# Kernel optimization log

Hardware: AMD Instinct MI355X
Metric: run time of the kernel (lower is better)

The kernel has to match this reference:

```python
import jax, jax.numpy as jnp
import numpy as np

N_HEADS = 4
LEAKY_SLOPE = 0.2


def setup_inputs() -> dict:
    key = jax.random.key(0)
    k1, k2, k3 = jax.random.split(key, 3)
    b, c, h, w = 8, 64, 128, 128
    z = jax.random.normal(k1, (b, c, h, w), dtype=jnp.float32)
    # torch.nn.Linear weights are (out_features, in_features); scale ~1/sqrt(fan_in)
    W_Q = jax.random.normal(k2, (c, c), dtype=jnp.float32) * 0.125
    W_K = jax.random.normal(k3, (c, c), dtype=jnp.float32) * 0.125
    return {"z": z, "W_Q": W_Q, "W_K": W_K}


def _axial_branch(z_perm_flat, z_raw_flat, W_Q, W_K, n_batch, seq, d_k, scale):
    # z_perm_flat: (n_batch, seq, c)  -- rearranged input fed to W_Q
    # z_raw_flat : (n_batch, seq, c)  -- raw memory-order reshape fed to W_K
    Q = jnp.matmul(z_perm_flat, W_Q.T).reshape(N_HEADS * n_batch, d_k, seq)
    V = jnp.matmul(z_raw_flat, W_K.T).reshape(N_HEADS * n_batch, d_k, seq)
    # QK-less scores: Q^T Q / sqrt(d_k)  -> (N, seq, seq)
    scores = jnp.einsum('nds,ndt->nst', Q, Q) * scale
    attn = jax.nn.softmax(scores, axis=-1)
    # right-multiply attention onto V, then LeakyReLU
    ctx = jnp.einsum('nds,nst->ndt', V, attn)
    return jax.nn.leaky_relu(ctx, negative_slope=LEAKY_SLOPE)


def reference(z, W_Q, W_K):
    b, c, h, w = z.shape
    d_k = c // N_HEADS
    scale = 1.0 / np.sqrt(d_k).astype(np.float32)

    # Branch 1 (attention over w): a = rearrange 'b c h w -> (b h) w c'
    a = jnp.transpose(z, (0, 2, 3, 1)).reshape(b * h, w, c)
    v1_in = z.reshape(b * h, w, c)  # raw reshape, as in the torch code
    context1 = _axial_branch(a, v1_in, W_Q, W_K, b * h, w, d_k, scale)

    # Branch 2 (attention over h): m = rearrange 'b c h w -> (b w) h c'
    m = jnp.transpose(z, (0, 3, 2, 1)).reshape(b * w, h, c)
    v2_in = z.reshape(b * w, h, c)  # raw reshape, as in the torch code
    context2 = _axial_branch(m, v2_in, W_Q, W_K, b * w, h, d_k, scale)

    context = context1 + context2  # requires h == w
    return context.reshape(b, c, h, w)
```

## Files before the change

kernel.cpp:

```cpp
#include <hip/hip_runtime.h>


typedef __attribute__((ext_vector_type(8))) short bh8;
typedef __attribute__((ext_vector_type(4))) float f32x4;
typedef unsigned short u16;
typedef unsigned int u32;

#define MFMA16(a,b,c) __builtin_amdgcn_mfma_f32_16x16x32_bf16(a,b,c,0,0,0)

#define AIMG_ST 72
#define QP_ST   40
#define V_ST    136
#define PT_ST   72

#define OFF_AH   0
#define OFF_AL   4608
#define OFF_PT   0
#define OFF_QP   18432
#define OFF_VH   28672
#define OFF_VL   33024
#define LDS_TOT  37376

__device__ __forceinline__ void split3(float f, u16& h, u16& l) {
    u32 u = __float_as_uint(f);
    u32 hf = u & 0xFFFF0000u;
    float r = f - __uint_as_float(hf);
    h = (u16)(hf >> 16);
    l = (u16)((__float_as_uint(r) + 0x8000u) >> 16);
}
__device__ __forceinline__ void split2pk(float f0, float f1, u32& hp, u32& lp) {
    u32 u0 = __float_as_uint(f0), u1 = __float_as_uint(f1);
    u32 h0 = u0 & 0xFFFF0000u,  h1 = u1 & 0xFFFF0000u;
    float r0 = f0 - __uint_as_float(h0);
    float r1 = f1 - __uint_as_float(h1);
    hp = (h0 >> 16) | h1;
    lp = ((__float_as_uint(r0) + 0x8000u) >> 16) | ((__float_as_uint(r1) + 0x8000u) & 0xFFFF0000u);
}
__device__ __forceinline__ float lrelu(float x) { return x > 0.f ? x : 0.2f * x; }

__global__ void split_w_kernel(const float* __restrict__ Wq,
                               const float* __restrict__ Wk,
                               u16* __restrict__ ws)
{
    const int i = blockIdx.x * 256 + threadIdx.x;
    const int j = i & 4095;
    const float f = (i < 4096) ? Wq[j] : Wk[j];
    const int base = (i < 4096) ? 0 : 8192;
    u16 h, l; split3(f, h, l);
    ws[base + j] = h;
    ws[base + 4096 + j] = l;
}

template<int MODE>
__device__ __forceinline__ void gemm_in(const u16* Ah, const u16* Al,
                                        bh8 h0a, bh8 h0b, bh8 l0a, bh8 l0b,
                                        bh8 h1a, bh8 h1b, bh8 l1a, bh8 l1b,
                                        u16* o0, u16* o1,
                                        int miQ, int niA, int lid, int quad)
{
    const int offA = (miQ*16 + lid)*AIMG_ST + quad*8;
    bh8 ah0 = *(const bh8*)(Ah + offA);
    bh8 ah1 = *(const bh8*)(Ah + offA + 32);
    bh8 al0 = *(const bh8*)(Al + offA);
    bh8 al1 = *(const bh8*)(Al + offA + 32);
    f32x4 acc0 = {0.f,0.f,0.f,0.f}, acc1 = {0.f,0.f,0.f,0.f};
    acc0 = MFMA16(ah0, h0a, acc0); acc0 = MFMA16(ah0, l0a, acc0); acc0 = MFMA16(al0, h0a, acc0);
    acc0 = MFMA16(ah1, h0b, acc0); acc0 = MFMA16(ah1, l0b, acc0); acc0 = MFMA16(al1, h0b, acc0);
    acc1 = MFMA16(ah0, h1a, acc1); acc1 = MFMA16(ah0, l1a, acc1); acc1 = MFMA16(al0, h1a, acc1);
    acc1 = MFMA16(ah1, h1b, acc1); acc1 = MFMA16(ah1, l1b, acc1); acc1 = MFMA16(al1, h1b, acc1);
    #pragma unroll
    for (int r = 0; r < 4; ++r) {
        const int l = miQ*16 + quad*4 + r;
        const int d = l >> 1;
        const int sbase = (l & 1) << 6;
        {
            const int s = sbase + (niA + 0)*16 + lid;
            u16 h, lo; split3(MODE == 0 ? 0.5f*acc0[r] : acc0[r], h, lo);
            if (MODE == 0) { o0[s*QP_ST + d] = h; o0[s*QP_ST + 16 + d] = lo; }
            else           { o0[d*V_ST + s] = h; o1[d*V_ST + s] = lo; }
        }
        {
            const int s = sbase + (niA + 1)*16 + lid;
            u16 h, lo; split3(MODE == 0 ? 0.5f*acc1[r] : acc1[r], h, lo);
            if (MODE == 0) { o0[s*QP_ST + d] = h; o0[s*QP_ST + 16 + d] = lo; }
            else           { o0[d*V_ST + s] = h; o1[d*V_ST + s] = lo; }
        }
    }
}

__device__ __forceinline__ void branch_attn(const u16* Qp, const u16* Vh, const u16* Vl,
                                            u16* PT, f32x4& cacc0, f32x4& cacc1,
                                            int w, int lid, int quad)
{
    const f32x4 z4 = {0.f, 0.f, 0.f, 0.f};
    cacc0 = z4; cacc1 = z4;
    for (int round = 0; round < 2; ++round) {
        const int rowS = (round*4 + w)*16 + lid;
        const u16* arow = Qp + rowS*QP_ST;
        bh8 a1 = *(const bh8*)(arow + quad*8);
        bh8 a2 = *(const bh8*)(arow + ((quad >= 2) ? (quad-2)*8 : 0));
        bh8 zzv = a2 ^ a2;
        a2 = (quad < 2) ? zzv : a2;
        f32x4 g[8];
        #pragma unroll
        for (int ti = 0; ti < 8; ++ti) {
            const u16* brow = Qp + (ti*16 + lid)*QP_ST;
            bh8 b1 = *(const bh8*)(brow + (quad & 1)*8);
            bh8 b2 = *(const bh8*)(brow + quad*8);
            f32x4 acc = z4;
            acc = MFMA16(a1, b1, acc);
            acc = MFMA16(a2, b2, acc);
            g[ti] = acc;
        }
        float sm[4] = {0.f, 0.f, 0.f, 0.f};
        #pragma unroll
        for (int ti = 0; ti < 8; ++ti)
        #pragma unroll
        for (int r = 0; r < 4; ++r) {
            const float p = __expf(g[ti][r]);
            g[ti][r] = p; sm[r] += p;
        }
        #pragma unroll
        for (int r = 0; r < 4; ++r) {
            float ss = sm[r];
            ss += __shfl_xor(ss, 1); ss += __shfl_xor(ss, 2);
            ss += __shfl_xor(ss, 4); ss += __shfl_xor(ss, 8);
            sm[r] = 1.0f / ss;
        }
        #pragma unroll
        for (int ti = 0; ti < 8; ++ti) {
            const u32 r0 = __float_as_uint(g[ti][0]*sm[0]) + 0x8000u;
            const u32 r1 = __float_as_uint(g[ti][1]*sm[1]) + 0x8000u;
            const u32 r2 = __float_as_uint(g[ti][2]*sm[2]) + 0x8000u;
            const u32 r3 = __float_as_uint(g[ti][3]*sm[3]) + 0x8000u;
            u32* dst = (u32*)(PT + (ti*16 + lid)*PT_ST + w*16 + quad*4);
            dst[0] = (r0 >> 16) | (r1 & 0xFFFF0000u);
            dst[1] = (r2 >> 16) | (r3 & 0xFFFF0000u);
        }
        __syncthreads();
        #pragma unroll
        for (int tj2 = 0; tj2 < 2; ++tj2) {
            const int tj = 2*w + tj2;
            f32x4 acc = tj2 ? cacc1 : cacc0;
            #pragma unroll
            for (int ks = 0; ks < 2; ++ks) {
                bh8 pa = *(const bh8*)(PT + (tj*16 + lid)*PT_ST + ks*32 + quad*8);
                const int vo = lid*V_ST + round*64 + ks*32 + quad*8;
                bh8 vh8 = *(const bh8*)(Vh + vo);
                bh8 vl8 = *(const bh8*)(Vl + vo);
                acc = MFMA16(pa, vh8, acc);
                acc = MFMA16(pa, vl8, acc);
            }
            if (tj2) cacc1 = acc; else cacc0 = acc;
        }
        __syncthreads();
    }
}

#define WOFF(n, ks) (((n)*16 + lid)*64 + (ks)*32 + quad*8)

__global__ __launch_bounds__(256, 4)
void axial_attn_mfma(const float* __restrict__ z, const u16* __restrict__ wsu,
                     float* __restrict__ out)
{
    __shared__ __align__(16) unsigned char lds[LDS_TOT];
    u16* const ptAh = (u16*)(lds + OFF_AH);
    u16* const ptAl = (u16*)(lds + OFF_AL);
    u16* const ptPT = (u16*)(lds + OFF_PT);
    u16* const ptQP = (u16*)(lds + OFF_QP);
    u16* const ptVH = (u16*)(lds + OFF_VH);
    u16* const ptVL = (u16*)(lds + OFF_VL);

    const int tid = threadIdx.x;
    const int w = tid >> 6, lane = tid & 63, quad = lane >> 4, lid = lane & 15;

    const int blk = blockIdx.x;
    const int j   = blk >> 3;
    const int xi  = ((blk & 7) << 4) | (j & 15);
    const int q   = (j >> 4) & 3;
    const int bi  = j >> 6;
    const int N   = (((bi << 7) | xi) << 2) | q;
    const size_t zbase = (size_t)bi << 20;

    const int ch0 = tid >> 5, l5 = tid & 31;
    const int vl0 = tid >> 4, vc0 = (tid & 15) << 2;

    float a1r[8], a2r[8];
    float4 v4[2];
    {
        const float* s1 = z + zbase + ((size_t)xi << 7) + (q << 5) + l5;
        const float* s2 = z + zbase + (((size_t)(q*32 + l5)) << 7) + xi;
        #pragma unroll
        for (int k = 0; k < 8; ++k)
            a1r[k] = s1[(size_t)(ch0 + 8*k) << 14];
        const float4* sv = (const float4*)(z + ((size_t)N << 11));
        v4[0] = sv[tid]; v4[1] = sv[tid + 256];
        #pragma unroll
        for (int k = 0; k < 8; ++k)
            a2r[k] = s2[(size_t)(ch0 + 8*k) << 14];
    }

    const int niA = (w & 1) * 2, miQ = w >> 1;
    const bh8 qh0a = *(const bh8*)(wsu +        WOFF(niA+0,0));
    const bh8 qh0b = *(const bh8*)(wsu +        WOFF(niA+0,1));
    const bh8 qh1a = *(const bh8*)(wsu +        WOFF(niA+1,0));
    const bh8 qh1b = *(const bh8*)(wsu +        WOFF(niA+1,1));
    const bh8 ql0a = *(const bh8*)(wsu + 4096 + WOFF(niA+0,0));
    const bh8 ql0b = *(const bh8*)(wsu + 4096 + WOFF(niA+0,1));
    const bh8 ql1a = *(const bh8*)(wsu + 4096 + WOFF(niA+1,0));
    const bh8 ql1b = *(const bh8*)(wsu + 4096 + WOFF(niA+1,1));

    #pragma unroll
    for (int k = 0; k < 8; ++k) {
        u16 h, lo; split3(a1r[k], h, lo);
        ptAh[l5*AIMG_ST + ch0 + 8*k] = h;
        ptAl[l5*AIMG_ST + ch0 + 8*k] = lo;
    }
    __syncthreads();
    gemm_in<0>(ptAh, ptAl, qh0a, qh0b, ql0a, ql0b, qh1a, qh1b, ql1a, ql1b,
               ptQP, nullptr, miQ, niA, lid, quad);
    __syncthreads();

    {
        const bh8 kh0a = *(const bh8*)(wsu +  8192 + WOFF(niA+0,0));
        const bh8 kh0b = *(const bh8*)(wsu +  8192 + WOFF(niA+0,1));
        const bh8 kh1a = *(const bh8*)(wsu +  8192 + WOFF(niA+1,0));
        const bh8 kh1b = *(const bh8*)(wsu +  8192 + WOFF(niA+1,1));
        const bh8 kl0a = *(const bh8*)(wsu + 12288 + WOFF(niA+0,0));
        const bh8 kl0b = *(const bh8*)(wsu + 12288 + WOFF(niA+0,1));
        const bh8 kl1a = *(const bh8*)(wsu + 12288 + WOFF(niA+1,0));
        const bh8 kl1b = *(const bh8*)(wsu + 12288 + WOFF(niA+1,1));
        #pragma unroll
        for (int k = 0; k < 2; ++k) {
            const float4 vv = v4[k];
            u32 hp0, lp0, hp1, lp1;
            split2pk(vv.x, vv.y, hp0, lp0);
            split2pk(vv.z, vv.w, hp1, lp1);
            u32* dh = (u32*)(ptAh + (vl0 + 16*k)*AIMG_ST + vc0);
            u32* dl = (u32*)(ptAl + (vl0 + 16*k)*AIMG_ST + vc0);
            dh[0] = hp0; dh[1] = hp1;
            dl[0] = lp0; dl[1] = lp1;
        }
        __syncthreads();
        gemm_in<1>(ptAh, ptAl, kh0a, kh0b, kl0a, kl0b, kh1a, kh1b, kl1a, kl1b,
                   ptVH, ptVL, miQ, niA, lid, quad);
    }
    __syncthreads();

    f32x4 c10, c11;
    branch_attn(ptQP, ptVH, ptVL, ptPT, c10, c11, w, lid, quad);

    #pragma unroll
    for (int k = 0; k < 8; ++k) {
        u16 h, lo; split3(a2r[k], h, lo);
        ptAh[l5*AIMG_ST + ch0 + 8*k] = h;
        ptAl[l5*AIMG_ST + ch0 + 8*k] = lo;
    }
    __syncthreads();
    gemm_in<0>(ptAh, ptAl, qh0a, qh0b, ql0a, ql0b, qh1a, qh1b, ql1a, ql1b,
               ptQP, nullptr, miQ, niA, lid, quad);
    __syncthreads();

    f32x4 c20, c21;
    branch_attn(ptQP, ptVH, ptVL, ptPT, c20, c21, w, lid, quad);

    float* obase = out + ((size_t)N << 11) + lid*128;
    #pragma unroll
    for (int tj2 = 0; tj2 < 2; ++tj2) {
        f32x4 a = tj2 ? c11 : c10;
        f32x4 b = tj2 ? c21 : c20;
        float4 ov;
        ov.x = lrelu(a[0]) + lrelu(b[0]);
        ov.y = lrelu(a[1]) + lrelu(b[1]);
        ov.z = lrelu(a[2]) + lrelu(b[2]);
        ov.w = lrelu(a[3]) + lrelu(b[3]);
        *(float4*)(obase + (2*w + tj2)*16 + quad*4) = ov;
    }
}

extern "C" void kernel_launch(void* const* d_in, const int* in_sizes, int n_in,
                              void* d_out, int out_size, void* d_ws, size_t ws_size,
                              hipStream_t stream) {
    const float* z  = (const float*)d_in[0];
    const float* Wq = (const float*)d_in[1];
    const float* Wk = (const float*)d_in[2];
    float* out = (float*)d_out;
    u16* ws = (u16*)d_ws;
    hipLaunchKernelGGL(split_w_kernel, dim3(32), dim3(256), 0, stream, Wq, Wk, ws);
    hipLaunchKernelGGL(axial_attn_mfma, dim3(4096), dim3(256), 0, stream, z, ws, out);
}
```

Measured before the change: 161.1 us.

## Drop V low-part split and restructure attention into per-wave score blocks with LDS atomics

V is now computed as a single bf16 (hi only) GEMM instead of the 3-term hi/lo split, halving V MFMAs and LDS storage. The attention is reorganized so each wave owns 32 query rows, computes all scores at once, writes P to a per-wave LDS scratch, and accumulates context with LDS float atomicAdd into a shared CTX buffer, removing the mid-attention block barriers. Weight fragments are reloaded per GEMM rather than held in registers, and the LDS footprint shrinks. The risks are reduced V precision and contention or latency from the many LDS atomics.

```diff
diff --git a/kernel.cpp b/kernel.cpp
--- a/kernel.cpp
+++ b/kernel.cpp
@@ -10,16 +10,17 @@
 
 #define AIMG_ST 72
 #define QP_ST   40
-#define V_ST    136
-#define PT_ST   72
-
+#define VH_ST   136
+#define PS_ST   40
+#define CTX_ST  132
+
+#define OFF_PS   0
 #define OFF_AH   0
 #define OFF_AL   4608
-#define OFF_PT   0
-#define OFF_QP   18432
-#define OFF_VH   28672
-#define OFF_VL   33024
-#define LDS_TOT  37376
+#define OFF_QP   10240
+#define OFF_VH   20480
+#define OFF_CTX  24832
+#define LDS_TOT  33280
 
 __device__ __forceinline__ void split3(float f, u16& h, u16& l) {
     u32 u = __float_as_uint(f);
@@ -28,13 +29,12 @@
     h = (u16)(hf >> 16);
     l = (u16)((__float_as_uint(r) + 0x8000u) >> 16);
 }
-__device__ __forceinline__ void split2pk(float f0, float f1, u32& hp, u32& lp) {
-    u32 u0 = __float_as_uint(f0), u1 = __float_as_uint(f1);
-    u32 h0 = u0 & 0xFFFF0000u,  h1 = u1 & 0xFFFF0000u;
-    float r0 = f0 - __uint_as_float(h0);
-    float r1 = f1 - __uint_as_float(h1);
-    hp = (h0 >> 16) | h1;
-    lp = ((__float_as_uint(r0) + 0x8000u) >> 16) | ((__float_as_uint(r1) + 0x8000u) & 0xFFFF0000u);
+__device__ __forceinline__ u16 rnbf(float f) {
+    return (u16)((__float_as_uint(f) + 0x8000u) >> 16);
+}
+__device__ __forceinline__ u32 pkrn(float f0, float f1) {
+    return ((__float_as_uint(f0) + 0x8000u) >> 16) |
+           ((__float_as_uint(f1) + 0x8000u) & 0xFFFF0000u);
 }
 __device__ __forceinline__ float lrelu(float x) { return x > 0.f ? x : 0.2f * x; }
 
@@ -51,12 +51,12 @@
     ws[base + 4096 + j] = l;
 }
 
-template<int MODE>
-__device__ __forceinline__ void gemm_in(const u16* Ah, const u16* Al,
-                                        bh8 h0a, bh8 h0b, bh8 l0a, bh8 l0b,
-                                        bh8 h1a, bh8 h1b, bh8 l1a, bh8 l1b,
-                                        u16* o0, u16* o1,
-                                        int miQ, int niA, int lid, int quad)
+#define WOFF(n, ks) (((n)*16 + lid)*64 + (ks)*32 + quad*8)
+
+__device__ __forceinline__ void gemm_q(const u16* Ah, const u16* Al,
+                                       bh8 h0a, bh8 h0b, bh8 l0a, bh8 l0b,
+                                       bh8 h1a, bh8 h1b, bh8 l1a, bh8 l1b,
+                                       u16* qp, int miQ, int niA, int lid, int quad)
 {
     const int offA = (miQ*16 + lid)*AIMG_ST + quad*8;
     bh8 ah0 = *(const bh8*)(Ah + offA);
@@ -73,106 +73,119 @@
         const int l = miQ*16 + quad*4 + r;
         const int d = l >> 1;
         const int sbase = (l & 1) << 6;
-        {
-            const int s = sbase + (niA + 0)*16 + lid;
-            u16 h, lo; split3(MODE == 0 ? 0.5f*acc0[r] : acc0[r], h, lo);
-            if (MODE == 0) { o0[s*QP_ST + d] = h; o0[s*QP_ST + 16 + d] = lo; }
-            else           { o0[d*V_ST + s] = h; o1[d*V_ST + s] = lo; }
+        u16 h, lo;
+        const int s0 = sbase + (niA + 0)*16 + lid;
+        split3(0.5f*acc0[r], h, lo);
+        qp[s0*QP_ST + d] = h; qp[s0*QP_ST + 16 + d] = lo;
+        const int s1 = sbase + (niA + 1)*16 + lid;
+        split3(0.5f*acc1[r], h, lo);
+        qp[s1*QP_ST + d] = h; qp[s1*QP_ST + 16 + d] = lo;
+    }
+}
+
+__device__ __forceinline__ void gemm_v(const u16* Ah,
+                                       bh8 h0a, bh8 h0b, bh8 h1a, bh8 h1b,
+                                       u16* vh, int miQ, int niA, int lid, int quad)
+{
+    const int offA = (miQ*16 + lid)*AIMG_ST + quad*8;
+    bh8 ah0 = *(const bh8*)(Ah + offA);
+    bh8 ah1 = *(const bh8*)(Ah + offA + 32);
+    f32x4 acc0 = {0.f,0.f,0.f,0.f}, acc1 = {0.f,0.f,0.f,0.f};
+    acc0 = MFMA16(ah0, h0a, acc0); acc0 = MFMA16(ah1, h0b, acc0);
+    acc1 = MFMA16(ah0, h1a, acc1); acc1 = MFMA16(ah1, h1b, acc1);
+    #pragma unroll
+    for (int r = 0; r < 4; ++r) {
+        const int l = miQ*16 + quad*4 + r;
+        const int d = l >> 1;
+        const int sbase = (l & 1) << 6;
+        vh[d*VH_ST + sbase + (niA + 0)*16 + lid] = rnbf(acc0[r]);
+        vh[d*VH_ST + sbase + (niA + 1)*16 + lid] = rnbf(acc1[r]);
+    }
+}
+
+__device__ __forceinline__ void branch_attn(const u16* Qp, const u16* Vh,
+                                            u16* PSw, float* CTX,
+                                            int w, int lid, int quad)
+{
+    f32x4 g[2][8];
+    bh8 a1[2], a2[2];
+    #pragma unroll
+    for (int st = 0; st < 2; ++st) {
+        const u16* arow = Qp + (32*w + st*16 + lid)*QP_ST;
+        a1[st] = *(const bh8*)(arow + quad*8);
+        bh8 t = *(const bh8*)(arow + ((quad >= 2) ? (quad-2)*8 : 0));
+        bh8 zz = t ^ t;
+        a2[st] = (quad < 2) ? zz : t;
+    }
+    #pragma unroll
+    for (int ti = 0; ti < 8; ++ti) {
+        const u16* brow = Qp + (ti*16 + lid)*QP_ST;
+        bh8 b1 = *(const bh8*)(brow + (quad & 1)*8);
+        bh8 b2 = *(const bh8*)(brow + quad*8);
+        #pragma unroll
+        for (int st = 0; st < 2; ++st) {
+            f32x4 acc = {0.f,0.f,0.f,0.f};
+            acc = MFMA16(a1[st], b1, acc);
+            acc = MFMA16(a2[st], b2, acc);
+            g[st][ti] = acc;
         }
-        {
-            const int s = sbase + (niA + 1)*16 + lid;
-            u16 h, lo; split3(MODE == 0 ? 0.5f*acc1[r] : acc1[r], h, lo);
-            if (MODE == 0) { o0[s*QP_ST + d] = h; o0[s*QP_ST + 16 + d] = lo; }
-            else           { o0[d*V_ST + s] = h; o1[d*V_ST + s] = lo; }
+    }
+    float inv[2][4];
+    #pragma unroll
+    for (int st = 0; st < 2; ++st)
+    #pragma unroll
+    for (int r = 0; r < 4; ++r) {
+        float s = 0.f;
+        #pragma unroll
+        for (int ti = 0; ti < 8; ++ti) {
+            const float p = __expf(g[st][ti][r]);
+            g[st][ti][r] = p; s += p;
         }
-    }
-}
-
-__device__ __forceinline__ void branch_attn(const u16* Qp, const u16* Vh, const u16* Vl,
-                                            u16* PT, f32x4& cacc0, f32x4& cacc1,
-                                            int w, int lid, int quad)
-{
-    const f32x4 z4 = {0.f, 0.f, 0.f, 0.f};
-    cacc0 = z4; cacc1 = z4;
-    for (int round = 0; round < 2; ++round) {
-        const int rowS = (round*4 + w)*16 + lid;
-        const u16* arow = Qp + rowS*QP_ST;
-        bh8 a1 = *(const bh8*)(arow + quad*8);
-        bh8 a2 = *(const bh8*)(arow + ((quad >= 2) ? (quad-2)*8 : 0));
-        bh8 zzv = a2 ^ a2;
-        a2 = (quad < 2) ? zzv : a2;
-        f32x4 g[8];
-        #pragma unroll
-        for (int ti = 0; ti < 8; ++ti) {
-            const u16* brow = Qp + (ti*16 + lid)*QP_ST;
-            bh8 b1 = *(const bh8*)(brow + (quad & 1)*8);
-            bh8 b2 = *(const bh8*)(brow + quad*8);
-            f32x4 acc = z4;
-            acc = MFMA16(a1, b1, acc);
-            acc = MFMA16(a2, b2, acc);
-            g[ti] = acc;
+        s += __shfl_xor(s, 1); s += __shfl_xor(s, 2);
+        s += __shfl_xor(s, 4); s += __shfl_xor(s, 8);
+        inv[st][r] = 1.0f / s;
+    }
+    const bh8 vfrag = *(const bh8*)(Vh + lid*VH_ST + 32*w + quad*8);
+    #pragma unroll
+    for (int p = 0; p < 4; ++p) {
+        #pragma unroll
+        for (int tii = 0; tii < 2; ++tii) {
+            const int ti = 2*p + tii;
+            #pragma unroll
+            for (int st = 0; st < 2; ++st) {
+                uint2 dv;
+                dv.x = pkrn(g[st][ti][0]*inv[st][0], g[st][ti][1]*inv[st][1]);
+                dv.y = pkrn(g[st][ti][2]*inv[st][2], g[st][ti][3]*inv[st][3]);
+                *(uint2*)(PSw + (tii*16 + lid)*PS_ST + st*16 + quad*4) = dv;
+            }
         }
-        float sm[4] = {0.f, 0.f, 0.f, 0.f};
-        #pragma unroll
-        for (int ti = 0; ti < 8; ++ti)
-        #pragma unroll
-        for (int r = 0; r < 4; ++r) {
-            const float p = __expf(g[ti][r]);
-            g[ti][r] = p; sm[r] += p;
+        #pragma unroll
+        for (int tii = 0; tii < 2; ++tii) {
+            const int ti = 2*p + tii;
+            const bh8 pf = *(const bh8*)(PSw + (tii*16 + lid)*PS_ST + quad*8);
+            f32x4 acc = {0.f,0.f,0.f,0.f};
+            acc = MFMA16(vfrag, pf, acc);
+            #pragma unroll
+            for (int r = 0; r < 4; ++r)
+                atomicAdd(CTX + (quad*4 + r)*CTX_ST + ti*16 + lid, acc[r]);
         }
-        #pragma unroll
-        for (int r = 0; r < 4; ++r) {
-            float ss = sm[r];
-            ss += __shfl_xor(ss, 1); ss += __shfl_xor(ss, 2);
-            ss += __shfl_xor(ss, 4); ss += __shfl_xor(ss, 8);
-            sm[r] = 1.0f / ss;
-        }
-        #pragma unroll
-        for (int ti = 0; ti < 8; ++ti) {
-            const u32 r0 = __float_as_uint(g[ti][0]*sm[0]) + 0x8000u;
-            const u32 r1 = __float_as_uint(g[ti][1]*sm[1]) + 0x8000u;
-            const u32 r2 = __float_as_uint(g[ti][2]*sm[2]) + 0x8000u;
-            const u32 r3 = __float_as_uint(g[ti][3]*sm[3]) + 0x8000u;
-            u32* dst = (u32*)(PT + (ti*16 + lid)*PT_ST + w*16 + quad*4);
-            dst[0] = (r0 >> 16) | (r1 & 0xFFFF0000u);
-            dst[1] = (r2 >> 16) | (r3 & 0xFFFF0000u);
-        }
-        __syncthreads();
-        #pragma unroll
-        for (int tj2 = 0; tj2 < 2; ++tj2) {
-            const int tj = 2*w + tj2;
-            f32x4 acc = tj2 ? cacc1 : cacc0;
-            #pragma unroll
-            for (int ks = 0; ks < 2; ++ks) {
-                bh8 pa = *(const bh8*)(PT + (tj*16 + lid)*PT_ST + ks*32 + quad*8);
-                const int vo = lid*V_ST + round*64 + ks*32 + quad*8;
-                bh8 vh8 = *(const bh8*)(Vh + vo);
-                bh8 vl8 = *(const bh8*)(Vl + vo);
-                acc = MFMA16(pa, vh8, acc);
-                acc = MFMA16(pa, vl8, acc);
-            }
-            if (tj2) cacc1 = acc; else cacc0 = acc;
-        }
-        __syncthreads();
-    }
-}
-
-#define WOFF(n, ks) (((n)*16 + lid)*64 + (ks)*32 + quad*8)
+    }
+}
 
 __global__ __launch_bounds__(256, 4)
 void axial_attn_mfma(const float* __restrict__ z, const u16* __restrict__ wsu,
                      float* __restrict__ out)
 {
     __shared__ __align__(16) unsigned char lds[LDS_TOT];
-    u16* const ptAh = (u16*)(lds + OFF_AH);
-    u16* const ptAl = (u16*)(lds + OFF_AL);
-    u16* const ptPT = (u16*)(lds + OFF_PT);
-    u16* const ptQP = (u16*)(lds + OFF_QP);
-    u16* const ptVH = (u16*)(lds + OFF_VH);
-    u16* const ptVL = (u16*)(lds + OFF_VL);
+    u16*   const ptAh = (u16*)(lds + OFF_AH);
+    u16*   const ptAl = (u16*)(lds + OFF_AL);
+    u16*   const ptQP = (u16*)(lds + OFF_QP);
+    u16*   const ptVH = (u16*)(lds + OFF_VH);
+    float* const ptCT = (float*)(lds + OFF_CTX);
 
     const int tid = threadIdx.x;
     const int w = tid >> 6, lane = tid & 63, quad = lane >> 4, lid = lane & 15;
+    u16* const ptPS = (u16*)(lds + OFF_PS) + w * 32 * PS_ST;
 
     const int blk = blockIdx.x;
     const int j   = blk >> 3;
@@ -184,6 +197,7 @@
 
     const int ch0 = tid >> 5, l5 = tid & 31;
     const int vl0 = tid >> 4, vc0 = (tid & 15) << 2;
+    const int miQ = w >> 1, niA = (w & 1) * 2;
 
     float a1r[8], a2r[8];
     float4 v4[2];
@@ -200,15 +214,11 @@
             a2r[k] = s2[(size_t)(ch0 + 8*k) << 14];
     }
 
-    const int niA = (w & 1) * 2, miQ = w >> 1;
-    const bh8 qh0a = *(const bh8*)(wsu +        WOFF(niA+0,0));
-    const bh8 qh0b = *(const bh8*)(wsu +        WOFF(niA+0,1));
-    const bh8 qh1a = *(const bh8*)(wsu +        WOFF(niA+1,0));
-    const bh8 qh1b = *(const bh8*)(wsu +        WOFF(niA+1,1));
-    const bh8 ql0a = *(const bh8*)(wsu + 4096 + WOFF(niA+0,0));
-    const bh8 ql0b = *(const bh8*)(wsu + 4096 + WOFF(niA+0,1));
-    const bh8 ql1a = *(const bh8*)(wsu + 4096 + WOFF(niA+1,0));
-    const bh8 ql1b = *(const bh8*)(wsu + 4096 + WOFF(niA+1,1));
+    float* const ctxp = ptCT + lid*CTX_ST + w*32 + quad*4;
+    {
+        const f32x4 zz = {0.f,0.f,0.f,0.f};
+        *(f32x4*)ctxp = zz; *(f32x4*)(ctxp + 16) = zz;
+    }
 
     #pragma unroll
     for (int k = 0; k < 8; ++k) {
@@ -217,38 +227,51 @@
         ptAl[l5*AIMG_ST + ch0 + 8*k] = lo;
     }
     __syncthreads();
-    gemm_in<0>(ptAh, ptAl, qh0a, qh0b, ql0a, ql0b, qh1a, qh1b, ql1a, ql1b,
-               ptQP, nullptr, miQ, niA, lid, quad);
-    __syncthreads();
-
-    {
-        const bh8 kh0a = *(const bh8*)(wsu +  8192 + WOFF(niA+0,0));
-        const bh8 kh0b = *(const bh8*)(wsu +  8192 + WOFF(niA+0,1));
-        const bh8 kh1a = *(const bh8*)(wsu +  8192 + WOFF(niA+1,0));
-        const bh8 kh1b = *(const bh8*)(wsu +  8192 + WOFF(niA+1,1));
-        const bh8 kl0a = *(const bh8*)(wsu + 12288 + WOFF(niA+0,0));
-        const bh8 kl0b = *(const bh8*)(wsu + 12288 + WOFF(niA+0,1));
-        const bh8 kl1a = *(const bh8*)(wsu + 12288 + WOFF(niA+1,0));
-        const bh8 kl1b = *(const bh8*)(wsu + 12288 + WOFF(niA+1,1));
-        #pragma unroll
-        for (int k = 0; k < 2; ++k) {
-            const float4 vv = v4[k];
-            u32 hp0, lp0, hp1, lp1;
-            split2pk(vv.x, vv.y, hp0, lp0);
-            split2pk(vv.z, vv.w, hp1, lp1);
-            u32* dh = (u32*)(ptAh + (vl0 + 16*k)*AIMG_ST + vc0);
-            u32* dl = (u32*)(ptAl + (vl0 + 16*k)*AIMG_ST + vc0);
-            dh[0] = hp0; dh[1] = hp1;
-            dl[0] = lp0; dl[1] = lp1;
-        }
-        __syncthreads();
-        gemm_in<1>(ptAh, ptAl, kh0a, kh0b, kl0a, kl0b, kh1a, kh1b, kl1a, kl1b,
-                   ptVH, ptVL, miQ, niA, lid, quad);
-    }
-    __syncthreads();
-
-    f32x4 c10, c11;
-    branch_attn(ptQP, ptVH, ptVL, ptPT, c10, c11, w, lid, quad);
+
+    {
+        const bh8 h0a = *(const bh8*)(wsu +        WOFF(niA+0,0));
+        const bh8 h0b = *(const bh8*)(wsu +        WOFF(niA+0,1));
+        const bh8 h1a = *(const bh8*)(wsu +        WOFF(niA+1,0));
+        const bh8 h1b = *(const bh8*)(wsu +        WOFF(niA+1,1));
+        const bh8 l0a = *(const bh8*)(wsu + 4096 + WOFF(niA+0,0));
+        const bh8 l0b = *(const bh8*)(wsu + 4096 + WOFF(niA+0,1));
+        const bh8 l1a = *(const bh8*)(wsu + 4096 + WOFF(niA+1,0));
+        const bh8 l1b = *(const bh8*)(wsu + 4096 + WOFF(niA+1,1));
+        gemm_q(ptAh, ptAl, h0a, h0b, l0a, l0b, h1a, h1b, l1a, l1b,
+               ptQP, miQ, niA, lid, quad);
+    }
+    __syncthreads();
+
+    #pragma unroll
+    for (int k = 0; k < 2; ++k) {
+        const float4 vv = v4[k];
+        uint2 dv;
+        dv.x = pkrn(vv.x, vv.y);
+        dv.y = pkrn(vv.z, vv.w);
+        *(uint2*)(ptAh + (vl0 + 16*k)*AIMG_ST + vc0) = dv;
+    }
+    __syncthreads();
+
+    {
+        const bh8 h0a = *(const bh8*)(wsu + 8192 + WOFF(niA+0,0));
+        const bh8 h0b = *(const bh8*)(wsu + 8192 + WOFF(niA+0,1));
+        const bh8 h1a = *(const bh8*)(wsu + 8192 + WOFF(niA+1,0));
+        const bh8 h1b = *(const bh8*)(wsu + 8192 + WOFF(niA+1,1));
+        gemm_v(ptAh, h0a, h0b, h1a, h1b, ptVH, miQ, niA, lid, quad);
+    }
+    __syncthreads();
+
+    branch_attn(ptQP, ptVH, ptPS, ptCT, w, lid, quad);
+    __syncthreads();
+
+    f32x4 c1a = *(f32x4*)ctxp;
+    f32x4 c1b = *(f32x4*)(ctxp + 16);
+    #pragma unroll
+    for (int r = 0; r < 4; ++r) { c1a[r] = lrelu(c1a[r]); c1b[r] = lrelu(c1b[r]); }
+    {
+        const f32x4 zz = {0.f,0.f,0.f,0.f};
+        *(f32x4*)ctxp = zz; *(f32x4*)(ctxp + 16) = zz;
+    }
 
     #pragma unroll
     for (int k = 0; k < 8; ++k) {
@@ -257,25 +280,34 @@
         ptAl[l5*AIMG_ST + ch0 + 8*k] = lo;
     }
     __syncthreads();
-    gemm_in<0>(ptAh, ptAl, qh0a, qh0b, ql0a, ql0b, qh1a, qh1b, ql1a, ql1b,
-               ptQP, nullptr, miQ, niA, lid, quad);
-    __syncthreads();
-
-    f32x4 c20, c21;
-    branch_attn(ptQP, ptVH, ptVL, ptPT, c20, c21, w, lid, quad);
-
-    float* obase = out + ((size_t)N << 11) + lid*128;
-    #pragma unroll
-    for (int tj2 = 0; tj2 < 2; ++tj2) {
-        f32x4 a = tj2 ? c11 : c10;
-        f32x4 b = tj2 ? c21 : c20;
-        float4 ov;
-        ov.x = lrelu(a[0]) + lrelu(b[0]);
-        ov.y = lrelu(a[1]) + lrelu(b[1]);
-        ov.z = lrelu(a[2]) + lrelu(b[2]);
-        ov.w = lrelu(a[3]) + lrelu(b[3]);
-        *(float4*)(obase + (2*w + tj2)*16 + quad*4) = ov;
-    }
+
+    {
+        const bh8 h0a = *(const bh8*)(wsu +        WOFF(niA+0,0));
+        const bh8 h0b = *(const bh8*)(wsu +        WOFF(niA+0,1));
+        const bh8 h1a = *(const bh8*)(wsu +        WOFF(niA+1,0));
+        const bh8 h1b = *(const bh8*)(wsu +        WOFF(niA+1,1));
+        const bh8 l0a = *(const bh8*)(wsu + 4096 + WOFF(niA+0,0));
+        const bh8 l0b = *(const bh8*)(wsu + 4096 + WOFF(niA+0,1));
+        const bh8 l1a = *(const bh8*)(wsu + 4096 + WOFF(niA+1,0));
+        const bh8 l1b = *(const bh8*)(wsu + 4096 + WOFF(niA+1,1));
+        gemm_q(ptAh, ptAl, h0a, h0b, l0a, l0b, h1a, h1b, l1a, l1b,
+               ptQP, miQ, niA, lid, quad);
+    }
+    __syncthreads();
+
+    branch_attn(ptQP, ptVH, ptPS, ptCT, w, lid, quad);
+    __syncthreads();
+
+    f32x4 c2a = *(f32x4*)ctxp;
+    f32x4 c2b = *(f32x4*)(ctxp + 16);
+    float* obase = out + ((size_t)N << 11) + lid*128 + w*32 + quad*4;
+    float4 o0, o1;
+    o0.x = c1a[0] + lrelu(c2a[0]); o0.y = c1a[1] + lrelu(c2a[1]);
+    o0.z = c1a[2] + lrelu(c2a[2]); o0.w = c1a[3] + lrelu(c2a[3]);
+    o1.x = c1b[0] + lrelu(c2b[0]); o1.y = c1b[1] + lrelu(c2b[1]);
+    o1.z = c1b[2] + lrelu(c2b[2]); o1.w = c1b[3] + lrelu(c2b[3]);
+    *(float4*)obase        = o0;
+    *(float4*)(obase + 16) = o1;
 }
 
 extern "C" void kernel_launch(void* const* d_in, const int* in_sizes, int n_in,
```

New measurement: 471.3 us. +192.5%, slower.
